# Kernel optimization log

Hardware: AMD Instinct MI355X
Metric: run time of the kernel (lower is better)

The kernel has to match this reference:

```python
import jax, jax.numpy as jnp
import numpy as np

NUM_SYMBOLS = 5
NUM_SUBCARRIERS = 33


def _dft_matrix(n):
    # Unitary DFT matrix: F[j,k] = exp(-2i*pi*j*k/n) / sqrt(n)
    omega = np.exp(-2j * np.pi / n)
    j, k = np.meshgrid(np.arange(n), np.arange(n))
    return (np.power(omega, j * k) / np.sqrt(n)).astype(np.complex64)


def setup_inputs() -> dict:
    key = jax.random.key(0)
    k1, k2 = jax.random.split(key)
    shape = (4096, NUM_SYMBOLS, 4, 4, NUM_SUBCARRIERS)  # (N, S, TXH, TXW, W)
    x_real = jax.random.normal(k1, shape, dtype=jnp.float32)
    x_imag = jax.random.normal(k2, shape, dtype=jnp.float32)
    F_sym = _dft_matrix(NUM_SYMBOLS)
    F_sub = _dft_matrix(NUM_SUBCARRIERS)
    return {
        "x_real": x_real,
        "x_imag": x_imag,
        "F_sym_real": jnp.asarray(F_sym.real, dtype=jnp.float32),
        "F_sym_imag": jnp.asarray(F_sym.imag, dtype=jnp.float32),
        "F_sub_real": jnp.asarray(F_sub.real, dtype=jnp.float32),
        "F_sub_imag": jnp.asarray(F_sub.imag, dtype=jnp.float32),
    }


def reference(x_real, x_imag, F_sym_real, F_sym_imag, F_sub_real, F_sub_imag):
    N, S, TXH, TXW, W = x_real.shape
    x = jax.lax.complex(x_real, x_imag).reshape(N, S, TXH * TXW, W)
    x = jnp.transpose(x, (0, 2, 1, 3))  # (N, A, S, W), A = TXH*TXW

    F_sym = jax.lax.complex(F_sym_real, F_sym_imag)  # (S, S)
    F_sub = jax.lax.complex(F_sub_real, F_sub_imag)  # (W, W)

    # 2D DFT across symbols (left) and subcarriers (right)
    X = jnp.einsum("st,natw->nasw", F_sym, x)
    X = jnp.einsum("nasw,wv->nasv", X, F_sub)

    # magnitude-square (power spectrum)
    X_mag_sq = (X.real * X.real + X.imag * X.imag).astype(jnp.complex64)

    # inverse 2D DFT (conjugate transposes) -> autocorrelation
    X = jnp.einsum("st,natw->nasw", F_sym.conj().T, X_mag_sq)
    X = jnp.einsum("nasw,wv->nasv", X, F_sub.conj().T)

    X = jnp.transpose(X, (0, 2, 1, 3))  # (N, S, A, W)
    return X.reshape(N, S, TXH, TXW, W)
```

## Files before the change

kernel.cpp:

```cpp
#include <hip/hip_runtime.h>

#define NS 5
#define NW 33
#define NA 16
#define SW 165
#define MPW 5
#define GM 20
#define TPM 11
#define CPT 3
#define THREADS 256

typedef float f2 __attribute__((ext_vector_type(2)));

__device__ __forceinline__ void cmac(f2& z, f2 x, f2 f) {
    asm("v_pk_fma_f32 %0, %1, %2, %0 op_sel:[0,0,0] op_sel_hi:[1,0,1]"
        : "+v"(z) : "v"(x), "v"(f));
    asm("v_pk_fma_f32 %0, %1, %2, %0 op_sel:[1,1,0] op_sel_hi:[0,1,1] neg_lo:[1,0,0]"
        : "+v"(z) : "v"(x), "v"(f));
}

__device__ __forceinline__ void cmacr(f2& z, f2 f, f2 Pp) {
    asm("v_pk_fma_f32 %0, %1, %2, %0 op_sel:[0,0,0] op_sel_hi:[1,1,1] neg_hi:[1,0,0]"
        : "+v"(z) : "v"(f), "v"(Pp));
}

__device__ __forceinline__ void pkfma(f2& z, f2 a, f2 b) {
    asm("v_pk_fma_f32 %0, %1, %2, %0 op_sel:[0,0,0] op_sel_hi:[1,1,1]"
        : "+v"(z) : "v"(a), "v"(b));
}

__global__ __launch_bounds__(THREADS, 4) void autocorr_kernel(
    const float* __restrict__ x_real, const float* __restrict__ x_imag,
    const float* __restrict__ Fsym_re, const float* __restrict__ Fsym_im,
    const float* __restrict__ Fsub_re, const float* __restrict__ Fsub_im,
    float* __restrict__ out, int NM, int write_complex)
{
    __shared__ f2 sFsym[NS * NS];
    __shared__ f2 sFsub[NW * NW];
    __shared__ f2 buf[GM][SW];

    const int tid = threadIdx.x;

    for (int i = tid; i < NW * NW; i += THREADS)
        sFsub[i] = (f2){Fsub_re[i], Fsub_im[i]};
    if (tid < NS * NS) sFsym[tid] = (f2){Fsym_re[tid], Fsym_im[tid]};
    __syncthreads();

    const int wave = tid >> 6;
    const int lane = tid & 63;
    const int Mw = blockIdx.x * GM + wave * MPW;
    f2* const wbuf = &buf[wave * MPW][0];

    for (int e = lane; e < MPW * SW; e += 64) {
        const int g = e / SW, r = e - g * SW;
        const int t = r / NW, w = r - t * NW;
        const int M = Mw + g;
        f2 val = (f2){0.f, 0.f};
        if (M < NM) {
            const int n = M >> 4, a = M & 15;
            const int off = ((n * NS + t) * NA + a) * NW + w;
            val = (f2){x_real[off], x_imag[off]};
        }
        wbuf[g * SW + w * NS + t] = val;
    }
    asm volatile("s_waitcnt lgkmcnt(0)" ::: "memory");

    const int g = lane / TPM;
    const int j = lane - g * TPM;
    const bool act = (lane < MPW * TPM);
    const int gg = act ? g : 0;
    const int M = Mw + g;
    const int c0 = 3 * j;

    f2 V[NS][CPT];
#pragma unroll
    for (int t = 0; t < NS; ++t)
#pragma unroll
        for (int k = 0; k < CPT; ++k) V[t][k] = (f2){0.f, 0.f};
    if (act) {
        const f2* bp = wbuf + gg * SW;
#pragma unroll 3
        for (int w = 0; w < NW; ++w) {
            f2 xc[NS];
#pragma unroll
            for (int t = 0; t < NS; ++t) xc[t] = bp[w * NS + t];
            f2 fv[CPT];
#pragma unroll
            for (int k = 0; k < CPT; ++k) fv[k] = sFsub[w * NW + c0 + k];
#pragma unroll
            for (int t = 0; t < NS; ++t)
#pragma unroll
                for (int k = 0; k < CPT; ++k)
                    cmac(V[t][k], xc[t], fv[k]);
        }
    }

    f2 T2[3][CPT];
#pragma unroll
    for (int p = 0; p < 3; ++p)
#pragma unroll
        for (int k = 0; k < CPT; ++k) T2[p][k] = (f2){0.f, 0.f};
    if (act) {
#pragma unroll
        for (int s = 0; s < NS; ++s) {
            f2 X[CPT];
#pragma unroll
            for (int k = 0; k < CPT; ++k) X[k] = (f2){0.f, 0.f};
#pragma unroll
            for (int t = 0; t < NS; ++t) {
                f2 f = sFsym[s * NS + t];
#pragma unroll
                for (int k = 0; k < CPT; ++k)
                    cmac(X[k], f, V[t][k]);
            }
#pragma unroll
            for (int k = 0; k < CPT; ++k) {
                const float Pv = X[k].x * X[k].x + X[k].y * X[k].y;
                const f2 Pp = (f2){Pv, Pv};
#pragma unroll
                for (int p = 0; p < 3; ++p)
                    cmacr(T2[p][k], sFsym[s * NS + p], Pp);
            }
        }
#pragma unroll
        for (int k = 0; k < CPT; ++k)
#pragma unroll
            for (int p = 0; p < 3; ++p)
                wbuf[gg * SW + (c0 + k) * 3 + p] = T2[p][k];
    }
    asm volatile("s_waitcnt lgkmcnt(0)" ::: "memory");

    if (act) {
        const f2* bp = wbuf + gg * SW;
        if (!write_complex) {
            f2 Ypk[3][CPT];
#pragma unroll
            for (int p = 0; p < 3; ++p)
#pragma unroll
                for (int k = 0; k < CPT; ++k) Ypk[p][k] = (f2){0.f, 0.f};
#pragma unroll 3
            for (int v = 0; v < NW; ++v) {
                f2 tc[3];
#pragma unroll
                for (int p = 0; p < 3; ++p) tc[p] = bp[v * 3 + p];
                f2 fw[CPT];
#pragma unroll
                for (int k = 0; k < CPT; ++k) fw[k] = sFsub[(c0 + k) * NW + v];
#pragma unroll
                for (int p = 0; p < 3; ++p)
#pragma unroll
                    for (int k = 0; k < CPT; ++k)
                        pkfma(Ypk[p][k], tc[p], fw[k]);
            }
            if (M < NM) {
                int n = M >> 4, a = M & 15;
                int obase = ((n * NS) * NA + a) * NW;
#pragma unroll
                for (int p = 0; p < 3; ++p) {
                    const int pp = (NS - p) % NS;
#pragma unroll
                    for (int k = 0; k < CPT; ++k) {
                        const int q = c0 + k;
                        const int qq = (NW - q) % NW;
                        const float Yr = Ypk[p][k].x + Ypk[p][k].y;
                        out[obase + p * (NA * NW) + q] = Yr;
                        out[obase + pp * (NA * NW) + qq] = Yr;
                    }
                }
            }
        } else {
            f2 Y[3][CPT];
#pragma unroll
            for (int p = 0; p < 3; ++p)
#pragma unroll
                for (int k = 0; k < CPT; ++k) Y[p][k] = (f2){0.f, 0.f};
            for (int v = 0; v < NW; ++v) {
                f2 tc[3];
#pragma unroll
                for (int p = 0; p < 3; ++p) tc[p] = bp[v * 3 + p];
                f2 fw[CPT];
#pragma unroll
                for (int k = 0; k < CPT; ++k) fw[k] = sFsub[(c0 + k) * NW + v];
#pragma unroll
                for (int p = 0; p < 3; ++p)
#pragma unroll
                    for (int k = 0; k < CPT; ++k) {
                        Y[p][k].x = fmaf(tc[p].x, fw[k].x, Y[p][k].x);
                        Y[p][k].x = fmaf(tc[p].y, fw[k].y, Y[p][k].x);
                        Y[p][k].y = fmaf(tc[p].y, fw[k].x, Y[p][k].y);
                        Y[p][k].y = fmaf(-tc[p].x, fw[k].y, Y[p][k].y);
                    }
            }
            if (M < NM) {
                int n = M >> 4, a = M & 15;
#pragma unroll
                for (int p = 0; p < 3; ++p) {
                    const int pp = (NS - p) % NS;
#pragma unroll
                    for (int k = 0; k < CPT; ++k) {
                        const int q = c0 + k;
                        const int qq = (NW - q) % NW;
                        ((float2*)out)[((n * NS + p) * NA + a) * NW + q] =
                            make_float2(Y[p][k].x, Y[p][k].y);
                        ((float2*)out)[((n * NS + pp) * NA + a) * NW + qq] =
                            make_float2(Y[p][k].x, -Y[p][k].y);
                    }
                }
            }
        }
    }
}

extern "C" void kernel_launch(void* const* d_in, const int* in_sizes, int n_in,
                              void* d_out, int out_size, void* d_ws, size_t ws_size,
                              hipStream_t stream) {
    const float* x_real  = (const float*)d_in[0];
    const float* x_imag  = (const float*)d_in[1];
    const float* Fsym_re = (const float*)d_in[2];
    const float* Fsym_im = (const float*)d_in[3];
    const float* Fsub_re = (const float*)d_in[4];
    const float* Fsub_im = (const float*)d_in[5];

    const int NM = in_sizes[0] / SW;
    const long long n_cplx = (long long)in_sizes[0];
    const int write_complex = ((long long)out_size >= 2 * n_cplx) ? 1 : 0;

    const int blocks = (NM + GM - 1) / GM;

    autocorr_kernel<<<blocks, THREADS, 0, stream>>>(
        x_real, x_imag, Fsym_re, Fsym_im, Fsub_re, Fsub_im,
        (float*)d_out, NM, write_complex);
}
```

Baseline: 187.8 us.

## Load inputs directly from global memory and shrink LDS buffer

Drops the cooperative staging of the input tile into shared memory and has each thread read its input values straight from global memory (through cache) inside the first DFT loop. The shared buffer is cut to hold only the intermediate T2 results, and launch bounds go from 4 to 6 waves per SIMD to raise occupancy. The cost is that the 11 threads of each group now issue redundant, strided global loads inside the inner loop, so performance leans on L1/L2 hits and may add latency. Fewer registers allowed per thread also risks spills.

```diff
diff --git a/kernel.cpp b/kernel.cpp
--- a/kernel.cpp
+++ b/kernel.cpp
@@ -4,6 +4,7 @@
 #define NW 33
 #define NA 16
 #define SW 165
+#define T2S 99
 #define MPW 5
 #define GM 20
 #define TPM 11
@@ -29,7 +30,7 @@
         : "+v"(z) : "v"(a), "v"(b));
 }
 
-__global__ __launch_bounds__(THREADS, 4) void autocorr_kernel(
+__global__ __launch_bounds__(THREADS, 6) void autocorr_kernel(
     const float* __restrict__ x_real, const float* __restrict__ x_imag,
     const float* __restrict__ Fsym_re, const float* __restrict__ Fsym_im,
     const float* __restrict__ Fsub_re, const float* __restrict__ Fsub_im,
@@ -37,7 +38,7 @@
 {
     __shared__ f2 sFsym[NS * NS];
     __shared__ f2 sFsub[NW * NW];
-    __shared__ f2 buf[GM][SW];
+    __shared__ f2 t2buf[GM * T2S];
 
     const int tid = threadIdx.x;
 
@@ -49,28 +50,18 @@
     const int wave = tid >> 6;
     const int lane = tid & 63;
     const int Mw = blockIdx.x * GM + wave * MPW;
-    f2* const wbuf = &buf[wave * MPW][0];
-
-    for (int e = lane; e < MPW * SW; e += 64) {
-        const int g = e / SW, r = e - g * SW;
-        const int t = r / NW, w = r - t * NW;
-        const int M = Mw + g;
-        f2 val = (f2){0.f, 0.f};
-        if (M < NM) {
-            const int n = M >> 4, a = M & 15;
-            const int off = ((n * NS + t) * NA + a) * NW + w;
-            val = (f2){x_real[off], x_imag[off]};
-        }
-        wbuf[g * SW + w * NS + t] = val;
-    }
-    asm volatile("s_waitcnt lgkmcnt(0)" ::: "memory");
 
     const int g = lane / TPM;
     const int j = lane - g * TPM;
     const bool act = (lane < MPW * TPM);
     const int gg = act ? g : 0;
-    const int M = Mw + g;
+    const int M = Mw + gg;
     const int c0 = 3 * j;
+
+    const int Ms = (M < NM) ? M : 0;
+    const int n = Ms >> 4, a = Ms & 15;
+    const float* __restrict__ xr = x_real + (n * NS * NA + a) * NW;
+    const float* __restrict__ xi = x_imag + (n * NS * NA + a) * NW;
 
     f2 V[NS][CPT];
 #pragma unroll
@@ -78,12 +69,12 @@
 #pragma unroll
         for (int k = 0; k < CPT; ++k) V[t][k] = (f2){0.f, 0.f};
     if (act) {
-        const f2* bp = wbuf + gg * SW;
 #pragma unroll 3
         for (int w = 0; w < NW; ++w) {
             f2 xc[NS];
 #pragma unroll
-            for (int t = 0; t < NS; ++t) xc[t] = bp[w * NS + t];
+            for (int t = 0; t < NS; ++t)
+                xc[t] = (f2){xr[t * (NA * NW) + w], xi[t * (NA * NW) + w]};
             f2 fv[CPT];
 #pragma unroll
             for (int k = 0; k < CPT; ++k) fv[k] = sFsub[w * NW + c0 + k];
@@ -122,16 +113,17 @@
                     cmacr(T2[p][k], sFsym[s * NS + p], Pp);
             }
         }
+        f2* const wb = &t2buf[(wave * MPW + gg) * T2S];
 #pragma unroll
         for (int k = 0; k < CPT; ++k)
 #pragma unroll
             for (int p = 0; p < 3; ++p)
-                wbuf[gg * SW + (c0 + k) * 3 + p] = T2[p][k];
+                wb[(c0 + k) * 3 + p] = T2[p][k];
     }
     asm volatile("s_waitcnt lgkmcnt(0)" ::: "memory");
 
     if (act) {
-        const f2* bp = wbuf + gg * SW;
+        const f2* bp = &t2buf[(wave * MPW + gg) * T2S];
         if (!write_complex) {
             f2 Ypk[3][CPT];
 #pragma unroll
@@ -153,7 +145,6 @@
                         pkfma(Ypk[p][k], tc[p], fw[k]);
             }
             if (M < NM) {
-                int n = M >> 4, a = M & 15;
                 int obase = ((n * NS) * NA + a) * NW;
 #pragma unroll
                 for (int p = 0; p < 3; ++p) {
@@ -192,7 +183,6 @@
                     }
             }
             if (M < NM) {
-                int n = M >> 4, a = M & 15;
 #pragma unroll
                 for (int p = 0; p < 3; ++p) {
                     const int pp = (NS - p) % NS;
```

Result: slower. 311.1 us (+65.7%).
